# Performance work log

Hardware: AMD Instinct MI355X
Metric: run time of the kernel (lower is better)

Reference implementation:

```python
import jax, jax.numpy as jnp
import numpy as np
import math

B, S, H, D = 1, 2048, 32, 128  # batch, local_seq (one ring block), num_heads, head_dim


def setup_inputs() -> dict:
    key = jax.random.key(0)
    kq, kk, kv = jax.random.split(key, 3)
    return {
        "query": jax.random.normal(kq, (B, S, H, D), dtype=jnp.float32),
        "key": jax.random.normal(kk, (B, S, H, D), dtype=jnp.float32),
        "value": jax.random.normal(kv, (B, S, H, D), dtype=jnp.float32),
    }


def reference(query, key, value):
    # RingAttention with world_size=1: a single ring step where q_block_idx == kv_block_idx,
    # i.e. standard causal attention on the local block. The online-softmax update from the
    # initial (output=0, lse=-inf) accumulator is the identity, so it is omitted.
    b, s, h, d = query.shape
    scale = 1.0 / math.sqrt(d)
    # [b, h, q, k] scores
    scores = jnp.einsum("bqhd,bkhd->bhqk", query, key) * scale
    causal = jnp.triu(jnp.ones((s, s), dtype=bool), k=1)  # True above diagonal -> masked
    scores = jnp.where(causal[None, None, :, :], -jnp.inf, scores)
    probs = jax.nn.softmax(scores, axis=-1)
    out = jnp.einsum("bhqk,bkhd->bqhd", probs, value)
    return out
```

## Files before the change

kernel.cpp:

```cpp
#include <hip/hip_runtime.h>
#include <hip/hip_bf16.h>
#include <stdint.h>

#define SEQ   2048
#define NHEAD 32
#define HDIM  128
#define RS    (NHEAD * HDIM)
#define KVBLK 64
#define QBLK  128
#define NTILES (SEQ / KVBLK)
#define TILE_BYTES 16384

typedef float  f32x16 __attribute__((ext_vector_type(16)));
typedef __bf16 bf16x8 __attribute__((ext_vector_type(8)));
typedef uint32_t u32;

__device__ __forceinline__ unsigned short f2bf(float f) {
  unsigned u = __builtin_bit_cast(unsigned, f);
  u += 0x7fffu + ((u >> 16) & 1u);
  return (unsigned short)(u >> 16);
}

__device__ __forceinline__ u32 packbf(float a, float b) {
  __bf16 x = (__bf16)a, y = (__bf16)b;
  unsigned short ux = __builtin_bit_cast(unsigned short, x);
  unsigned short uy = __builtin_bit_cast(unsigned short, y);
  return (u32)ux | ((u32)uy << 16);
}

__device__ __forceinline__ void gld16(const void* g, void* l) {
  __builtin_amdgcn_global_load_lds(
      (const __attribute__((address_space(1))) unsigned int*)g,
      (__attribute__((address_space(3))) unsigned int*)l, 16, 0, 0);
}

__global__ __launch_bounds__(256) void prepass_kernel(
    const float* __restrict__ K, const float* __restrict__ V,
    char* __restrict__ wsK, char* __restrict__ wsV) {
  const int tid = threadIdx.x;
  const int t   = blockIdx.x & (NTILES - 1);
  const int h   = blockIdx.x >> 5;
  const int kv0 = t * KVBLK;
  char* kd = wsK + (size_t)(h * NTILES + t) * TILE_BYTES;
  char* vd = wsV + (size_t)(h * NTILES + t) * TILE_BYTES;

  {
    const int c  = tid & 15;
    const int kr = tid >> 4;
#pragma unroll
    for (int ki = 0; ki < 4; ++ki) {
      const int kk = kr + ki * 16;
      const float* kp = K + (size_t)(kv0 + kk) * RS + h * HDIM + c * 8;
      float4 x0 = *(const float4*)kp;
      float4 x1 = *(const float4*)(kp + 4);
      uint32_t u0 = f2bf(x0.x) | ((uint32_t)f2bf(x0.y) << 16);
      uint32_t u1 = f2bf(x0.z) | ((uint32_t)f2bf(x0.w) << 16);
      uint32_t u2 = f2bf(x1.x) | ((uint32_t)f2bf(x1.y) << 16);
      uint32_t u3 = f2bf(x1.z) | ((uint32_t)f2bf(x1.w) << 16);
      const uint32_t byte = (uint32_t)(kk * 256) + (((uint32_t)(c * 16)) ^ (uint32_t)((kk & 15) << 4));
      *(uint4*)(kd + byte) = make_uint4(u0, u1, u2, u3);
    }
  }
  {
    const int d0  = (tid & 31) * 4;
    const int kk0 = (tid >> 5) * 8;
    float vv[8][4];
#pragma unroll
    for (int r = 0; r < 8; ++r) {
      const float* vp = V + (size_t)(kv0 + kk0 + r) * RS + h * HDIM + d0;
      float4 x = *(const float4*)vp;
      vv[r][0] = x.x; vv[r][1] = x.y; vv[r][2] = x.z; vv[r][3] = x.w;
    }
#pragma unroll
    for (int i = 0; i < 4; ++i) {
      const int d = d0 + i;
      uint32_t p0 = f2bf(vv[0][i]) | ((uint32_t)f2bf(vv[1][i]) << 16);
      uint32_t p1 = f2bf(vv[2][i]) | ((uint32_t)f2bf(vv[3][i]) << 16);
      uint32_t p2 = f2bf(vv[4][i]) | ((uint32_t)f2bf(vv[5][i]) << 16);
      uint32_t p3 = f2bf(vv[6][i]) | ((uint32_t)f2bf(vv[7][i]) << 16);
      const uint32_t byte = (uint32_t)(d * 128) + (((uint32_t)(kk0 * 2)) ^ (uint32_t)((d & 7) << 4));
      *(uint4*)(vd + byte) = make_uint4(p0, p1, p2, p3);
    }
  }
}

__global__ __launch_bounds__(256, 2) void fattn_main(
    const float* __restrict__ Q, const char* __restrict__ wsK,
    const char* __restrict__ wsV, float* __restrict__ O) {
  const int tid  = threadIdx.x;
  const int w    = tid >> 6;
  const int lane = tid & 63;
  const int n    = lane & 31;
  const int hh   = lane >> 5;

  const int bid  = blockIdx.x;
  const int b2   = bid & 255;
  const int vid  = (b2 & 7) * 32 + (b2 >> 3);
  const int head = vid >> 3;
  const int jj   = vid & 7;
  const int qb   = (bid < 256) ? (15 - jj) : jj;
  const int q0   = qb * QBLK;
  const int ntile  = 2 * qb + 2;
  const int diag_t = 2 * qb + (w >> 1);

  __shared__ __align__(16) char smem[65536];
  auto Kbuf = [&](int b) { return smem + b * 32768; };
  auto Vbuf = [&](int b) { return smem + b * 32768 + 16384; };

  const float qscale = 0.088388347648318447f * 1.4426950408889634f;

  const int qrow = q0 + w * 32 + n;

  bf16x8 bq[8];
  {
    const float* qp = Q + (size_t)qrow * RS + head * HDIM + hh * 8;
#pragma unroll
    for (int ks = 0; ks < 8; ++ks) {
      float4 v0 = *(const float4*)(qp + ks * 16);
      float4 v1 = *(const float4*)(qp + ks * 16 + 4);
      bf16x8 a;
      a[0] = (__bf16)(v0.x * qscale); a[1] = (__bf16)(v0.y * qscale);
      a[2] = (__bf16)(v0.z * qscale); a[3] = (__bf16)(v0.w * qscale);
      a[4] = (__bf16)(v1.x * qscale); a[5] = (__bf16)(v1.y * qscale);
      a[6] = (__bf16)(v1.z * qscale); a[7] = (__bf16)(v1.w * qscale);
      bq[ks] = a;
    }
  }

  f32x16 accO[4];
#pragma unroll
  for (int i = 0; i < 4; ++i) accO[i] = (f32x16)(0.f);
  float m_run  = -1e30f;
  float l_part = 0.f;

  const char* kbase = wsK + (size_t)head * NTILES * TILE_BYTES;
  const char* vbase = wsV + (size_t)head * NTILES * TILE_BYTES;
  const bool  doK   = (w < 2);
  const char* sbase = doK ? kbase : vbase;
  const int   half  = (w & 1) * 8192;

  auto stage = [&](int buf, int t) {
    const char* src = sbase + (size_t)t * TILE_BYTES + half + lane * 16;
    char* dst = (doK ? Kbuf(buf) : Vbuf(buf)) + half;
#pragma unroll
    for (int i = 0; i < 8; ++i) gld16(src + i * 1024, dst + i * 1024);
  };

  stage(0, 0);
  asm volatile("s_waitcnt vmcnt(0)" ::: "memory");
  __builtin_amdgcn_sched_barrier(0);
  __syncthreads();

  for (int t = 0; t < ntile; ++t) {
    const int cur = t & 1;
    if (t + 1 < ntile) stage(cur ^ 1, t + 1);

    if (t <= diag_t) {
      const char* Kc = Kbuf(cur);
      const char* Vc = Vbuf(cur);

      f32x16 sc[2];
      __builtin_amdgcn_s_setprio(1);
#pragma unroll
      for (int kt = 0; kt < 2; ++kt) {
        f32x16 acc = (f32x16)(0.f);
        const int key = kt * 32 + n;
        const uint32_t rowb = (uint32_t)(key * 256);
        const uint32_t swz  = (uint32_t)((key & 15) << 4);
#pragma unroll
        for (int ks = 0; ks < 8; ++ks) {
          const uint32_t byte = rowb + (((uint32_t)(ks * 32 + hh * 16)) ^ swz);
          bf16x8 kf = *(const bf16x8*)(Kc + byte);
          acc = __builtin_amdgcn_mfma_f32_32x32x16_bf16(kf, bq[ks], acc, 0, 0, 0);
        }
        sc[kt] = acc;
      }
      __builtin_amdgcn_s_setprio(0);

      if (t == diag_t) {
        const int kv0 = t * KVBLK;
#pragma unroll
        for (int kt = 0; kt < 2; ++kt)
#pragma unroll
          for (int r = 0; r < 16; ++r) {
            const int keyg = kv0 + kt * 32 + (r & 3) + 8 * (r >> 2) + 4 * hh;
            if (keyg > qrow) sc[kt][r] = -1e30f;
          }
      }

      float mx = -1e30f;
#pragma unroll
      for (int kt = 0; kt < 2; ++kt)
#pragma unroll
        for (int r = 0; r < 16; ++r) mx = fmaxf(mx, sc[kt][r]);
      mx = fmaxf(mx, __shfl_xor(mx, 32, 64));

      if (__any(mx - m_run > 11.0f)) {
        const float mn = fmaxf(m_run, mx);
        const float al = exp2f(m_run - mn);
        m_run = mn;
        l_part *= al;
#pragma unroll
        for (int r = 0; r < 16; ++r) {
          const float ar = __shfl(al, (r & 3) + 8 * (r >> 2) + 4 * hh, 64);
#pragma unroll
          for (int nt = 0; nt < 4; ++nt) accO[nt][r] *= ar;
        }
      }

      float ls = 0.f;
#pragma unroll
      for (int kt = 0; kt < 2; ++kt)
#pragma unroll
        for (int r = 0; r < 16; ++r) {
          const float p = exp2f(sc[kt][r] - m_run);
          sc[kt][r] = p;
          ls += p;
        }
      l_part += ls;

      u32 ua[2][4], ub[2][4];
#pragma unroll
      for (int kt = 0; kt < 2; ++kt)
#pragma unroll
        for (int i = 0; i < 4; ++i) {
          ua[kt][i] = packbf(sc[kt][4 * i],     sc[kt][4 * i + 1]);
          ub[kt][i] = packbf(sc[kt][4 * i + 2], sc[kt][4 * i + 3]);
        }

      u32 ra[2][2], rb[2][2];
#pragma unroll
      for (int kt = 0; kt < 2; ++kt)
#pragma unroll
        for (int q = 0; q < 2; ++q) {
          ra[kt][q] = __shfl_xor(hh ? ua[kt][2 * q] : ua[kt][2 * q + 1], 32, 64);
          rb[kt][q] = __shfl_xor(hh ? ub[kt][2 * q] : ub[kt][2 * q + 1], 32, 64);
        }

      __builtin_amdgcn_s_setprio(1);
#pragma unroll
      for (int s = 0; s < 4; ++s) {
        const int kt = s >> 1, q = s & 1;
        u32 af32[4];
        af32[0] = hh ? ra[kt][q] : ua[kt][2 * q];
        af32[1] = hh ? rb[kt][q] : ub[kt][2 * q];
        af32[2] = hh ? ua[kt][2 * q + 1] : ra[kt][q];
        af32[3] = hh ? ub[kt][2 * q + 1] : rb[kt][q];
        bf16x8 af = __builtin_bit_cast(bf16x8, *(uint4*)af32);
#pragma unroll
        for (int nt = 0; nt < 4; ++nt) {
          const int d = nt * 32 + n;
          const uint32_t byte = (uint32_t)(d * 128) +
              (((uint32_t)(s * 32 + hh * 16)) ^ (uint32_t)((d & 7) << 4));
          bf16x8 vf = *(const bf16x8*)(Vc + byte);
          accO[nt] = __builtin_amdgcn_mfma_f32_32x32x16_bf16(af, vf, accO[nt], 0, 0, 0);
        }
      }
      __builtin_amdgcn_s_setprio(0);
    }

    asm volatile("s_waitcnt vmcnt(0) lgkmcnt(0)" ::: "memory");
    __builtin_amdgcn_sched_barrier(0);
    __syncthreads();
  }

  const float lf  = l_part + __shfl_xor(l_part, 32, 64);
  const float inv = 1.0f / lf;
  float* ob = O + (size_t)(q0 + w * 32) * RS + head * HDIM;
#pragma unroll
  for (int r = 0; r < 16; ++r) {
    const int m = (r & 3) + 8 * (r >> 2) + 4 * hh;
    const float im = __shfl(inv, m, 64);
#pragma unroll
    for (int nt = 0; nt < 4; ++nt)
      ob[(size_t)m * RS + nt * 32 + n] = accO[nt][r] * im;
  }
}

extern "C" void kernel_launch(void* const* d_in, const int* in_sizes, int n_in,
                              void* d_out, int out_size, void* d_ws, size_t ws_size,
                              hipStream_t stream) {
  const float* q = (const float*)d_in[0];
  const float* k = (const float*)d_in[1];
  const float* v = (const float*)d_in[2];
  float* o = (float*)d_out;
  char* wsK = (char*)d_ws;
  char* wsV = wsK + (size_t)NHEAD * NTILES * TILE_BYTES;
  hipLaunchKernelGGL(prepass_kernel, dim3(NHEAD * NTILES), dim3(256), 0, stream,
                     k, v, wsK, wsV);
  hipLaunchKernelGGL(fattn_main, dim3(512), dim3(256), 0, stream, q, wsK, wsV, o);
}
```

Measured before the change: 88.42 us.

## Software-pipeline attention loop so tile t-1's PV overlaps tile t's QK

Restructures the KV loop into a two-stage software pipeline. Each iteration issues QK^T for tile t, then PV for tile t-1 using packed probabilities held over in registers, then the softmax for tile t. V staging moves one tile later to match. The goal is to interleave independent MFMA work with the exp and shuffle softmax work so matrix units stay busy. In exchange it adds an extra loop iteration, keeps 16 more live registers for the held-over probabilities, and changes the staging order, which may raise register pressure and lower occupancy.

```diff
diff --git a/kernel.cpp b/kernel.cpp
--- a/kernel.cpp
+++ b/kernel.cpp
@@ -108,7 +108,6 @@
   auto Vbuf = [&](int b) { return smem + b * 32768 + 16384; };
 
   const float qscale = 0.088388347648318447f * 1.4426950408889634f;
-
   const int qrow = q0 + w * 32 + n;
 
   bf16x8 bq[8];
@@ -132,6 +131,7 @@
   for (int i = 0; i < 4; ++i) accO[i] = (f32x16)(0.f);
   float m_run  = -1e30f;
   float l_part = 0.f;
+  u32 pa[4][4];
 
   const char* kbase = wsK + (size_t)head * NTILES * TILE_BYTES;
   const char* vbase = wsV + (size_t)head * NTILES * TILE_BYTES;
@@ -146,20 +146,23 @@
     for (int i = 0; i < 8; ++i) gld16(src + i * 1024, dst + i * 1024);
   };
 
-  stage(0, 0);
+  if (doK) stage(0, 0);
   asm volatile("s_waitcnt vmcnt(0)" ::: "memory");
   __builtin_amdgcn_sched_barrier(0);
   __syncthreads();
 
-  for (int t = 0; t < ntile; ++t) {
-    const int cur = t & 1;
-    if (t + 1 < ntile) stage(cur ^ 1, t + 1);
-
-    if (t <= diag_t) {
-      const char* Kc = Kbuf(cur);
-      const char* Vc = Vbuf(cur);
-
-      f32x16 sc[2];
+  for (int t = 0; t <= ntile; ++t) {
+    if (t < ntile) {
+      if (doK) { if (t + 1 < ntile) stage((t + 1) & 1, t + 1); }
+      else     stage(t & 1, t);
+    }
+
+    const bool doqk = (t < ntile) && (t <= diag_t);
+    const bool dopv = (t > 0) && (t - 1 <= diag_t);
+
+    f32x16 sc[2];
+    if (doqk) {
+      const char* Kc = Kbuf(t & 1);
       __builtin_amdgcn_s_setprio(1);
 #pragma unroll
       for (int kt = 0; kt < 2; ++kt) {
@@ -176,77 +179,14 @@
         sc[kt] = acc;
       }
       __builtin_amdgcn_s_setprio(0);
-
-      if (t == diag_t) {
-        const int kv0 = t * KVBLK;
-#pragma unroll
-        for (int kt = 0; kt < 2; ++kt)
-#pragma unroll
-          for (int r = 0; r < 16; ++r) {
-            const int keyg = kv0 + kt * 32 + (r & 3) + 8 * (r >> 2) + 4 * hh;
-            if (keyg > qrow) sc[kt][r] = -1e30f;
-          }
-      }
-
-      float mx = -1e30f;
-#pragma unroll
-      for (int kt = 0; kt < 2; ++kt)
-#pragma unroll
-        for (int r = 0; r < 16; ++r) mx = fmaxf(mx, sc[kt][r]);
-      mx = fmaxf(mx, __shfl_xor(mx, 32, 64));
-
-      if (__any(mx - m_run > 11.0f)) {
-        const float mn = fmaxf(m_run, mx);
-        const float al = exp2f(m_run - mn);
-        m_run = mn;
-        l_part *= al;
-#pragma unroll
-        for (int r = 0; r < 16; ++r) {
-          const float ar = __shfl(al, (r & 3) + 8 * (r >> 2) + 4 * hh, 64);
-#pragma unroll
-          for (int nt = 0; nt < 4; ++nt) accO[nt][r] *= ar;
-        }
-      }
-
-      float ls = 0.f;
-#pragma unroll
-      for (int kt = 0; kt < 2; ++kt)
-#pragma unroll
-        for (int r = 0; r < 16; ++r) {
-          const float p = exp2f(sc[kt][r] - m_run);
-          sc[kt][r] = p;
-          ls += p;
-        }
-      l_part += ls;
-
-      u32 ua[2][4], ub[2][4];
-#pragma unroll
-      for (int kt = 0; kt < 2; ++kt)
-#pragma unroll
-        for (int i = 0; i < 4; ++i) {
-          ua[kt][i] = packbf(sc[kt][4 * i],     sc[kt][4 * i + 1]);
-          ub[kt][i] = packbf(sc[kt][4 * i + 2], sc[kt][4 * i + 3]);
-        }
-
-      u32 ra[2][2], rb[2][2];
-#pragma unroll
-      for (int kt = 0; kt < 2; ++kt)
-#pragma unroll
-        for (int q = 0; q < 2; ++q) {
-          ra[kt][q] = __shfl_xor(hh ? ua[kt][2 * q] : ua[kt][2 * q + 1], 32, 64);
-          rb[kt][q] = __shfl_xor(hh ? ub[kt][2 * q] : ub[kt][2 * q + 1], 32, 64);
-        }
-
+    }
+
+    if (dopv) {
+      const char* Vc = Vbuf((t - 1) & 1);
       __builtin_amdgcn_s_setprio(1);
 #pragma unroll
       for (int s = 0; s < 4; ++s) {
-        const int kt = s >> 1, q = s & 1;
-        u32 af32[4];
-        af32[0] = hh ? ra[kt][q] : ua[kt][2 * q];
-        af32[1] = hh ? rb[kt][q] : ub[kt][2 * q];
-        af32[2] = hh ? ua[kt][2 * q + 1] : ra[kt][q];
-        af32[3] = hh ? ub[kt][2 * q + 1] : rb[kt][q];
-        bf16x8 af = __builtin_bit_cast(bf16x8, *(uint4*)af32);
+        bf16x8 af = __builtin_bit_cast(bf16x8, *(uint4*)pa[s]);
 #pragma unroll
         for (int nt = 0; nt < 4; ++nt) {
           const int d = nt * 32 + n;
@@ -259,9 +199,80 @@
       __builtin_amdgcn_s_setprio(0);
     }
 
-    asm volatile("s_waitcnt vmcnt(0) lgkmcnt(0)" ::: "memory");
-    __builtin_amdgcn_sched_barrier(0);
-    __syncthreads();
+    if (doqk) {
+      if (t == diag_t) {
+        const int kv0 = t * KVBLK;
+#pragma unroll
+        for (int kt = 0; kt < 2; ++kt)
+#pragma unroll
+          for (int r = 0; r < 16; ++r) {
+            const int keyg = kv0 + kt * 32 + (r & 3) + 8 * (r >> 2) + 4 * hh;
+            if (keyg > qrow) sc[kt][r] = -1e30f;
+          }
+      }
+
+      float mx = -1e30f;
+#pragma unroll
+      for (int kt = 0; kt < 2; ++kt)
+#pragma unroll
+        for (int r = 0; r < 16; ++r) mx = fmaxf(mx, sc[kt][r]);
+      mx = fmaxf(mx, __shfl_xor(mx, 32, 64));
+
+      if (__any(mx - m_run > 11.0f)) {
+        const float mn = fmaxf(m_run, mx);
+        const float al = exp2f(m_run - mn);
+        m_run = mn;
+        l_part *= al;
+#pragma unroll
+        for (int r = 0; r < 16; ++r) {
+          const float ar = __shfl(al, (r & 3) + 8 * (r >> 2) + 4 * hh, 64);
+#pragma unroll
+          for (int nt = 0; nt < 4; ++nt) accO[nt][r] *= ar;
+        }
+      }
+
+      float ls = 0.f;
+#pragma unroll
+      for (int kt = 0; kt < 2; ++kt)
+#pragma unroll
+        for (int r = 0; r < 16; ++r) {
+          const float p = exp2f(sc[kt][r] - m_run);
+          sc[kt][r] = p;
+          ls += p;
+        }
+      l_part += ls;
+
+      u32 ua[2][4], ub[2][4];
+#pragma unroll
+      for (int kt = 0; kt < 2; ++kt)
+#pragma unroll
+        for (int i = 0; i < 4; ++i) {
+          ua[kt][i] = packbf(sc[kt][4 * i],     sc[kt][4 * i + 1]);
+          ub[kt][i] = packbf(sc[kt][4 * i + 2], sc[kt][4 * i + 3]);
+        }
+      u32 ra[2][2], rb[2][2];
+#pragma unroll
+      for (int kt = 0; kt < 2; ++kt)
+#pragma unroll
+        for (int q = 0; q < 2; ++q) {
+          ra[kt][q] = __shfl_xor(hh ? ua[kt][2 * q] : ua[kt][2 * q + 1], 32, 64);
+          rb[kt][q] = __shfl_xor(hh ? ub[kt][2 * q] : ub[kt][2 * q + 1], 32, 64);
+        }
+#pragma unroll
+      for (int s = 0; s < 4; ++s) {
+        const int kt = s >> 1, q = s & 1;
+        pa[s][0] = hh ? ra[kt][q] : ua[kt][2 * q];
+        pa[s][1] = hh ? rb[kt][q] : ub[kt][2 * q];
+        pa[s][2] = hh ? ua[kt][2 * q + 1] : ra[kt][q];
+        pa[s][3] = hh ? ub[kt][2 * q + 1] : rb[kt][q];
+      }
+    }
+
+    if (t < ntile) {
+      asm volatile("s_waitcnt vmcnt(0) lgkmcnt(0)" ::: "memory");
+      __builtin_amdgcn_sched_barrier(0);
+      __syncthreads();
+    }
   }
 
   const float lf  = l_part + __shfl_xor(l_part, 32, 64);
```

After: 97.57 us. +10.3%, slower.

## Stage K/V tiles through registers into a single LDS buffer

Applied to the files above, without the earlier changes.

Replaces the double-buffered direct global-to-LDS loads with register-staged prefetch. The next tile is loaded into VGPRs while the current tile is computed, then written to a single 32KB LDS buffer after a barrier. This halves LDS use, which may allow more blocks per CU, but it costs extra VGPRs and adds a second barrier per tile. Output stores also become nontemporal.

```diff
diff --git a/kernel.cpp b/kernel.cpp
--- a/kernel.cpp
+++ b/kernel.cpp
@@ -26,12 +26,6 @@
   unsigned short ux = __builtin_bit_cast(unsigned short, x);
   unsigned short uy = __builtin_bit_cast(unsigned short, y);
   return (u32)ux | ((u32)uy << 16);
-}
-
-__device__ __forceinline__ void gld16(const void* g, void* l) {
-  __builtin_amdgcn_global_load_lds(
-      (const __attribute__((address_space(1))) unsigned int*)g,
-      (__attribute__((address_space(3))) unsigned int*)l, 16, 0, 0);
 }
 
 __global__ __launch_bounds__(256) void prepass_kernel(
@@ -103,12 +97,11 @@
   const int ntile  = 2 * qb + 2;
   const int diag_t = 2 * qb + (w >> 1);
 
-  __shared__ __align__(16) char smem[65536];
-  auto Kbuf = [&](int b) { return smem + b * 32768; };
-  auto Vbuf = [&](int b) { return smem + b * 32768 + 16384; };
+  __shared__ __align__(16) char smem[32768];
+  char* Ksm = smem;
+  char* Vsm = smem + 16384;
 
   const float qscale = 0.088388347648318447f * 1.4426950408889634f;
-
   const int qrow = q0 + w * 32 + n;
 
   bf16x8 bq[8];
@@ -139,26 +132,26 @@
   const char* sbase = doK ? kbase : vbase;
   const int   half  = (w & 1) * 8192;
 
-  auto stage = [&](int buf, int t) {
+  uint4 streg[8];
+  auto stage_load = [&](int t) {
     const char* src = sbase + (size_t)t * TILE_BYTES + half + lane * 16;
-    char* dst = (doK ? Kbuf(buf) : Vbuf(buf)) + half;
-#pragma unroll
-    for (int i = 0; i < 8; ++i) gld16(src + i * 1024, dst + i * 1024);
+#pragma unroll
+    for (int i = 0; i < 8; ++i) streg[i] = *(const uint4*)(src + i * 1024);
   };
-
-  stage(0, 0);
-  asm volatile("s_waitcnt vmcnt(0)" ::: "memory");
-  __builtin_amdgcn_sched_barrier(0);
+  auto stage_write = [&]() {
+    char* dst = (doK ? Ksm : Vsm) + half + lane * 16;
+#pragma unroll
+    for (int i = 0; i < 8; ++i) *(uint4*)(dst + i * 1024) = streg[i];
+  };
+
+  stage_load(0);
+  stage_write();
   __syncthreads();
 
   for (int t = 0; t < ntile; ++t) {
-    const int cur = t & 1;
-    if (t + 1 < ntile) stage(cur ^ 1, t + 1);
+    if (t + 1 < ntile) stage_load(t + 1);
 
     if (t <= diag_t) {
-      const char* Kc = Kbuf(cur);
-      const char* Vc = Vbuf(cur);
-
       f32x16 sc[2];
       __builtin_amdgcn_s_setprio(1);
 #pragma unroll
@@ -170,7 +163,7 @@
 #pragma unroll
         for (int ks = 0; ks < 8; ++ks) {
           const uint32_t byte = rowb + (((uint32_t)(ks * 32 + hh * 16)) ^ swz);
-          bf16x8 kf = *(const bf16x8*)(Kc + byte);
+          bf16x8 kf = *(const bf16x8*)(Ksm + byte);
           acc = __builtin_amdgcn_mfma_f32_32x32x16_bf16(kf, bq[ks], acc, 0, 0, 0);
         }
         sc[kt] = acc;
@@ -227,7 +220,6 @@
           ua[kt][i] = packbf(sc[kt][4 * i],     sc[kt][4 * i + 1]);
           ub[kt][i] = packbf(sc[kt][4 * i + 2], sc[kt][4 * i + 3]);
         }
-
       u32 ra[2][2], rb[2][2];
 #pragma unroll
       for (int kt = 0; kt < 2; ++kt)
@@ -252,16 +244,21 @@
           const int d = nt * 32 + n;
           const uint32_t byte = (uint32_t)(d * 128) +
               (((uint32_t)(s * 32 + hh * 16)) ^ (uint32_t)((d & 7) << 4));
-          bf16x8 vf = *(const bf16x8*)(Vc + byte);
+          bf16x8 vf = *(const bf16x8*)(Vsm + byte);
           accO[nt] = __builtin_amdgcn_mfma_f32_32x32x16_bf16(af, vf, accO[nt], 0, 0, 0);
         }
       }
       __builtin_amdgcn_s_setprio(0);
     }
 
-    asm volatile("s_waitcnt vmcnt(0) lgkmcnt(0)" ::: "memory");
-    __builtin_amdgcn_sched_barrier(0);
-    __syncthreads();
+    if (t + 1 < ntile) {
+      asm volatile("s_waitcnt lgkmcnt(0)" ::: "memory");
+      __builtin_amdgcn_sched_barrier(0);
+      __builtin_amdgcn_s_barrier();
+      __builtin_amdgcn_sched_barrier(0);
+      stage_write();
+      __syncthreads();
+    }
   }
 
   const float lf  = l_part + __shfl_xor(l_part, 32, 64);
@@ -273,7 +270,7 @@
     const float im = __shfl(inv, m, 64);
 #pragma unroll
     for (int nt = 0; nt < 4; ++nt)
-      ob[(size_t)m * RS + nt * 32 + n] = accO[nt][r] * im;
+      __builtin_nontemporal_store(accO[nt][r] * im, &ob[(size_t)m * RS + nt * 32 + n]);
   }
 }
 
```

New measurement: 147.4 us. 1.67x slower.

## Use single-wave blocks loading MFMA-fragment-ordered K/V directly from global memory

Applied to the files above, without the earlier changes.

The prepass now writes K and V in a layout where each lane's MFMA operand fragment is a contiguous 16-byte chunk. The main kernel drops LDS staging, double buffering and block barriers, and runs one 64-thread wave per 32-query tile (2048 blocks) that reads its K/V fragments straight into registers. This removes LDS traffic and __syncthreads stalls, and lets each wave stop at its own causal diagonal. In exchange, each wave re-reads K/V from global or L2 with no sharing across waves, and the large register arrays for K/V fragments may lower occupancy or expose load latency.

```diff
diff --git a/kernel.cpp b/kernel.cpp
--- a/kernel.cpp
+++ b/kernel.cpp
@@ -7,7 +7,6 @@
 #define HDIM  128
 #define RS    (NHEAD * HDIM)
 #define KVBLK 64
-#define QBLK  128
 #define NTILES (SEQ / KVBLK)
 #define TILE_BYTES 16384
 
@@ -26,12 +25,6 @@
   unsigned short ux = __builtin_bit_cast(unsigned short, x);
   unsigned short uy = __builtin_bit_cast(unsigned short, y);
   return (u32)ux | ((u32)uy << 16);
-}
-
-__device__ __forceinline__ void gld16(const void* g, void* l) {
-  __builtin_amdgcn_global_load_lds(
-      (const __attribute__((address_space(1))) unsigned int*)g,
-      (__attribute__((address_space(3))) unsigned int*)l, 16, 0, 0);
 }
 
 __global__ __launch_bounds__(256) void prepass_kernel(
@@ -57,7 +50,8 @@
       uint32_t u1 = f2bf(x0.z) | ((uint32_t)f2bf(x0.w) << 16);
       uint32_t u2 = f2bf(x1.x) | ((uint32_t)f2bf(x1.y) << 16);
       uint32_t u3 = f2bf(x1.z) | ((uint32_t)f2bf(x1.w) << 16);
-      const uint32_t byte = (uint32_t)(kk * 256) + (((uint32_t)(c * 16)) ^ (uint32_t)((kk & 15) << 4));
+      const int kt = kk >> 5, n = kk & 31, ks = c >> 1, hh = c & 1;
+      const uint32_t byte = (uint32_t)((kt * 8 + ks) * 1024 + (hh * 32 + n) * 16);
       *(uint4*)(kd + byte) = make_uint4(u0, u1, u2, u3);
     }
   }
@@ -71,6 +65,7 @@
       float4 x = *(const float4*)vp;
       vv[r][0] = x.x; vv[r][1] = x.y; vv[r][2] = x.z; vv[r][3] = x.w;
     }
+    const int s = kk0 >> 4, hh = (kk0 >> 3) & 1;
 #pragma unroll
     for (int i = 0; i < 4; ++i) {
       const int d = d0 + i;
@@ -78,38 +73,28 @@
       uint32_t p1 = f2bf(vv[2][i]) | ((uint32_t)f2bf(vv[3][i]) << 16);
       uint32_t p2 = f2bf(vv[4][i]) | ((uint32_t)f2bf(vv[5][i]) << 16);
       uint32_t p3 = f2bf(vv[6][i]) | ((uint32_t)f2bf(vv[7][i]) << 16);
-      const uint32_t byte = (uint32_t)(d * 128) + (((uint32_t)(kk0 * 2)) ^ (uint32_t)((d & 7) << 4));
+      const int nt = d >> 5;
+      const uint32_t byte = (uint32_t)((s * 4 + nt) * 1024 + (hh * 32 + (d & 31)) * 16);
       *(uint4*)(vd + byte) = make_uint4(p0, p1, p2, p3);
     }
   }
 }
 
-__global__ __launch_bounds__(256, 2) void fattn_main(
+__global__ __launch_bounds__(64, 2) void fattn_main(
     const float* __restrict__ Q, const char* __restrict__ wsK,
     const char* __restrict__ wsV, float* __restrict__ O) {
-  const int tid  = threadIdx.x;
-  const int w    = tid >> 6;
-  const int lane = tid & 63;
+  const int lane = threadIdx.x;
   const int n    = lane & 31;
   const int hh   = lane >> 5;
 
   const int bid  = blockIdx.x;
-  const int b2   = bid & 255;
-  const int vid  = (b2 & 7) * 32 + (b2 >> 3);
-  const int head = vid >> 3;
-  const int jj   = vid & 7;
-  const int qb   = (bid < 256) ? (15 - jj) : jj;
-  const int q0   = qb * QBLK;
-  const int ntile  = 2 * qb + 2;
-  const int diag_t = 2 * qb + (w >> 1);
-
-  __shared__ __align__(16) char smem[65536];
-  auto Kbuf = [&](int b) { return smem + b * 32768; };
-  auto Vbuf = [&](int b) { return smem + b * 32768 + 16384; };
+  const int k    = bid >> 3;
+  const int head = (bid & 7) * 4 + (k & 3);
+  const int qi   = 63 - (k >> 2);
+  const int ntile = (qi >> 1) + 1;
+  const int qrow  = qi * 32 + n;
 
   const float qscale = 0.088388347648318447f * 1.4426950408889634f;
-
-  const int qrow = q0 + w * 32 + n;
 
   bf16x8 bq[8];
   {
@@ -133,140 +118,115 @@
   float m_run  = -1e30f;
   float l_part = 0.f;
 
-  const char* kbase = wsK + (size_t)head * NTILES * TILE_BYTES;
-  const char* vbase = wsV + (size_t)head * NTILES * TILE_BYTES;
-  const bool  doK   = (w < 2);
-  const char* sbase = doK ? kbase : vbase;
-  const int   half  = (w & 1) * 8192;
-
-  auto stage = [&](int buf, int t) {
-    const char* src = sbase + (size_t)t * TILE_BYTES + half + lane * 16;
-    char* dst = (doK ? Kbuf(buf) : Vbuf(buf)) + half;
-#pragma unroll
-    for (int i = 0; i < 8; ++i) gld16(src + i * 1024, dst + i * 1024);
-  };
-
-  stage(0, 0);
-  asm volatile("s_waitcnt vmcnt(0)" ::: "memory");
-  __builtin_amdgcn_sched_barrier(0);
-  __syncthreads();
+  const char* kimg = wsK + (size_t)head * NTILES * TILE_BYTES;
+  const char* vimg = wsV + (size_t)head * NTILES * TILE_BYTES;
 
   for (int t = 0; t < ntile; ++t) {
-    const int cur = t & 1;
-    if (t + 1 < ntile) stage(cur ^ 1, t + 1);
-
-    if (t <= diag_t) {
-      const char* Kc = Kbuf(cur);
-      const char* Vc = Vbuf(cur);
-
-      f32x16 sc[2];
-      __builtin_amdgcn_s_setprio(1);
-#pragma unroll
-      for (int kt = 0; kt < 2; ++kt) {
-        f32x16 acc = (f32x16)(0.f);
-        const int key = kt * 32 + n;
-        const uint32_t rowb = (uint32_t)(key * 256);
-        const uint32_t swz  = (uint32_t)((key & 15) << 4);
-#pragma unroll
-        for (int ks = 0; ks < 8; ++ks) {
-          const uint32_t byte = rowb + (((uint32_t)(ks * 32 + hh * 16)) ^ swz);
-          bf16x8 kf = *(const bf16x8*)(Kc + byte);
-          acc = __builtin_amdgcn_mfma_f32_32x32x16_bf16(kf, bq[ks], acc, 0, 0, 0);
+    const char* kb = kimg + (size_t)t * TILE_BYTES + lane * 16;
+    uint4 kld[16];
+#pragma unroll
+    for (int i = 0; i < 16; ++i) kld[i] = *(const uint4*)(kb + i * 1024);
+
+    f32x16 sc[2];
+    __builtin_amdgcn_s_setprio(1);
+#pragma unroll
+    for (int kt = 0; kt < 2; ++kt) {
+      f32x16 acc = (f32x16)(0.f);
+#pragma unroll
+      for (int ks = 0; ks < 8; ++ks) {
+        bf16x8 kf = __builtin_bit_cast(bf16x8, kld[kt * 8 + ks]);
+        acc = __builtin_amdgcn_mfma_f32_32x32x16_bf16(kf, bq[ks], acc, 0, 0, 0);
+      }
+      sc[kt] = acc;
+    }
+    __builtin_amdgcn_s_setprio(0);
+
+    const char* vb = vimg + (size_t)t * TILE_BYTES + lane * 16;
+    uint4 vld[16];
+#pragma unroll
+    for (int i = 0; i < 16; ++i) vld[i] = *(const uint4*)(vb + i * 1024);
+
+    if (t == ntile - 1) {
+      const int kv0 = t * KVBLK;
+#pragma unroll
+      for (int kt = 0; kt < 2; ++kt)
+#pragma unroll
+        for (int r = 0; r < 16; ++r) {
+          const int keyg = kv0 + kt * 32 + (r & 3) + 8 * (r >> 2) + 4 * hh;
+          if (keyg > qrow) sc[kt][r] = -1e30f;
         }
-        sc[kt] = acc;
-      }
-      __builtin_amdgcn_s_setprio(0);
-
-      if (t == diag_t) {
-        const int kv0 = t * KVBLK;
-#pragma unroll
-        for (int kt = 0; kt < 2; ++kt)
-#pragma unroll
-          for (int r = 0; r < 16; ++r) {
-            const int keyg = kv0 + kt * 32 + (r & 3) + 8 * (r >> 2) + 4 * hh;
-            if (keyg > qrow) sc[kt][r] = -1e30f;
-          }
-      }
-
-      float mx = -1e30f;
-#pragma unroll
-      for (int kt = 0; kt < 2; ++kt)
-#pragma unroll
-        for (int r = 0; r < 16; ++r) mx = fmaxf(mx, sc[kt][r]);
-      mx = fmaxf(mx, __shfl_xor(mx, 32, 64));
-
-      if (__any(mx - m_run > 11.0f)) {
-        const float mn = fmaxf(m_run, mx);
-        const float al = exp2f(m_run - mn);
-        m_run = mn;
-        l_part *= al;
-#pragma unroll
-        for (int r = 0; r < 16; ++r) {
-          const float ar = __shfl(al, (r & 3) + 8 * (r >> 2) + 4 * hh, 64);
-#pragma unroll
-          for (int nt = 0; nt < 4; ++nt) accO[nt][r] *= ar;
-        }
-      }
-
-      float ls = 0.f;
-#pragma unroll
-      for (int kt = 0; kt < 2; ++kt)
-#pragma unroll
-        for (int r = 0; r < 16; ++r) {
-          const float p = exp2f(sc[kt][r] - m_run);
-          sc[kt][r] = p;
-          ls += p;
-        }
-      l_part += ls;
-
-      u32 ua[2][4], ub[2][4];
-#pragma unroll
-      for (int kt = 0; kt < 2; ++kt)
-#pragma unroll
-        for (int i = 0; i < 4; ++i) {
-          ua[kt][i] = packbf(sc[kt][4 * i],     sc[kt][4 * i + 1]);
-          ub[kt][i] = packbf(sc[kt][4 * i + 2], sc[kt][4 * i + 3]);
-        }
-
-      u32 ra[2][2], rb[2][2];
-#pragma unroll
-      for (int kt = 0; kt < 2; ++kt)
-#pragma unroll
-        for (int q = 0; q < 2; ++q) {
-          ra[kt][q] = __shfl_xor(hh ? ua[kt][2 * q] : ua[kt][2 * q + 1], 32, 64);
-          rb[kt][q] = __shfl_xor(hh ? ub[kt][2 * q] : ub[kt][2 * q + 1], 32, 64);
-        }
-
-      __builtin_amdgcn_s_setprio(1);
-#pragma unroll
-      for (int s = 0; s < 4; ++s) {
-        const int kt = s >> 1, q = s & 1;
-        u32 af32[4];
-        af32[0] = hh ? ra[kt][q] : ua[kt][2 * q];
-        af32[1] = hh ? rb[kt][q] : ub[kt][2 * q];
-        af32[2] = hh ? ua[kt][2 * q + 1] : ra[kt][q];
-        af32[3] = hh ? ub[kt][2 * q + 1] : rb[kt][q];
-        bf16x8 af = __builtin_bit_cast(bf16x8, *(uint4*)af32);
-#pragma unroll
-        for (int nt = 0; nt < 4; ++nt) {
-          const int d = nt * 32 + n;
-          const uint32_t byte = (uint32_t)(d * 128) +
-              (((uint32_t)(s * 32 + hh * 16)) ^ (uint32_t)((d & 7) << 4));
-          bf16x8 vf = *(const bf16x8*)(Vc + byte);
-          accO[nt] = __builtin_amdgcn_mfma_f32_32x32x16_bf16(af, vf, accO[nt], 0, 0, 0);
-        }
-      }
-      __builtin_amdgcn_s_setprio(0);
-    }
-
-    asm volatile("s_waitcnt vmcnt(0) lgkmcnt(0)" ::: "memory");
-    __builtin_amdgcn_sched_barrier(0);
-    __syncthreads();
+    }
+
+    float mx = -1e30f;
+#pragma unroll
+    for (int kt = 0; kt < 2; ++kt)
+#pragma unroll
+      for (int r = 0; r < 16; ++r) mx = fmaxf(mx, sc[kt][r]);
+    mx = fmaxf(mx, __shfl_xor(mx, 32, 64));
+
+    if (__any(mx - m_run > 11.0f)) {
+      const float mn = fmaxf(m_run, mx);
+      const float al = exp2f(m_run - mn);
+      m_run = mn;
+      l_part *= al;
+#pragma unroll
+      for (int r = 0; r < 16; ++r) {
+        const float ar = __shfl(al, (r & 3) + 8 * (r >> 2) + 4 * hh, 64);
+#pragma unroll
+        for (int nt = 0; nt < 4; ++nt) accO[nt][r] *= ar;
+      }
+    }
+
+    float ls = 0.f;
+#pragma unroll
+    for (int kt = 0; kt < 2; ++kt)
+#pragma unroll
+      for (int r = 0; r < 16; ++r) {
+        const float p = exp2f(sc[kt][r] - m_run);
+        sc[kt][r] = p;
+        ls += p;
+      }
+    l_part += ls;
+
+    u32 ua[2][4], ub[2][4];
+#pragma unroll
+    for (int kt = 0; kt < 2; ++kt)
+#pragma unroll
+      for (int i = 0; i < 4; ++i) {
+        ua[kt][i] = packbf(sc[kt][4 * i],     sc[kt][4 * i + 1]);
+        ub[kt][i] = packbf(sc[kt][4 * i + 2], sc[kt][4 * i + 3]);
+      }
+    u32 ra[2][2], rb[2][2];
+#pragma unroll
+    for (int kt = 0; kt < 2; ++kt)
+#pragma unroll
+      for (int q = 0; q < 2; ++q) {
+        ra[kt][q] = __shfl_xor(hh ? ua[kt][2 * q] : ua[kt][2 * q + 1], 32, 64);
+        rb[kt][q] = __shfl_xor(hh ? ub[kt][2 * q] : ub[kt][2 * q + 1], 32, 64);
+      }
+
+    __builtin_amdgcn_s_setprio(1);
+#pragma unroll
+    for (int s = 0; s < 4; ++s) {
+      const int kt = s >> 1, q = s & 1;
+      u32 af32[4];
+      af32[0] = hh ? ra[kt][q] : ua[kt][2 * q];
+      af32[1] = hh ? rb[kt][q] : ub[kt][2 * q];
+      af32[2] = hh ? ua[kt][2 * q + 1] : ra[kt][q];
+      af32[3] = hh ? ub[kt][2 * q + 1] : rb[kt][q];
+      bf16x8 af = __builtin_bit_cast(bf16x8, *(uint4*)af32);
+#pragma unroll
+      for (int nt = 0; nt < 4; ++nt) {
+        bf16x8 vf = __builtin_bit_cast(bf16x8, vld[s * 4 + nt]);
+        accO[nt] = __builtin_amdgcn_mfma_f32_32x32x16_bf16(af, vf, accO[nt], 0, 0, 0);
+      }
+    }
+    __builtin_amdgcn_s_setprio(0);
   }
 
   const float lf  = l_part + __shfl_xor(l_part, 32, 64);
   const float inv = 1.0f / lf;
-  float* ob = O + (size_t)(q0 + w * 32) * RS + head * HDIM;
+  float* ob = O + (size_t)(qi * 32) * RS + head * HDIM;
 #pragma unroll
   for (int r = 0; r < 16; ++r) {
     const int m = (r & 3) + 8 * (r >> 2) + 4 * hh;
@@ -288,5 +248,5 @@
   char* wsV = wsK + (size_t)NHEAD * NTILES * TILE_BYTES;
   hipLaunchKernelGGL(prepass_kernel, dim3(NHEAD * NTILES), dim3(256), 0, stream,
                      k, v, wsK, wsV);
-  hipLaunchKernelGGL(fattn_main, dim3(512), dim3(256), 0, stream, q, wsK, wsV, o);
-}
+  hipLaunchKernelGGL(fattn_main, dim3(2048), dim3(64), 0, stream, q, wsK, wsV, o);
+}
```

Result: no change. 89.10 us (+0.8%).
